# Optimization experiments

Measured on AMD Instinct MI355X. Metric: run time of the kernel, lower is better.

## Reference

```python
import jax, jax.numpy as jnp
import numpy as np

B = 16384      # batch
IN = 512       # input width
G, F, O = 64, 24, 16      # hidden: groups, fan_in, group_out (width = G*O = 1024)
GO_G, GO_F, GO_O = 4, 48, 16  # output layer: 4 groups x 16 = 64 outputs


def setup_inputs() -> dict:
    key = jax.random.key(0)
    ks = jax.random.split(key, 13)
    # total columns available (concat of input + all prior hidden layers)
    tot = [IN, IN + G * O, IN + 2 * G * O, IN + 3 * G * O]  # 512,1536,2560,3584
    scale = 0.1
    return {
        "x": jax.random.normal(ks[0], (B, IN), jnp.float32),
        "W1": jax.random.normal(ks[1], (G, F, O), jnp.float32) * scale,
        "b1": jnp.zeros((G, O), jnp.float32),
        "W2": jax.random.normal(ks[2], (G, F, O), jnp.float32) * scale,
        "b2": jnp.zeros((G, O), jnp.float32),
        "W3": jax.random.normal(ks[3], (G, F, O), jnp.float32) * scale,
        "b3": jnp.zeros((G, O), jnp.float32),
        "Wo": jax.random.normal(ks[4], (GO_G, GO_F, GO_O), jnp.float32) * scale,
        "bo": jnp.zeros((GO_G, GO_O), jnp.float32),
        "idx1": jax.random.randint(ks[5], (G, F), 0, tot[0], jnp.int32),
        "idx2": jax.random.randint(ks[6], (G, F), 0, tot[1], jnp.int32),
        "idx3": jax.random.randint(ks[7], (G, F), 0, tot[2], jnp.int32),
        "idxo": jax.random.randint(ks[8], (GO_G, GO_F), 0, tot[3], jnp.int32),
    }


def _group_layer(acc, idx, W, b, act):
    # acc: [B, P] concat of all prior layer outputs; idx: [G, F] column coords
    g = acc[:, idx]                               # [B, G, F] irregular gather
    h = jnp.einsum('bgf,gfo->bgo', g, W) + b      # many tiny dense sublayers
    h = act(h)
    return h.reshape(h.shape[0], -1)              # concat groups -> [B, G*O]


def reference(x, W1, b1, W2, b2, W3, b3, Wo, bo, idx1, idx2, idx3, idxo):
    acc = x
    for idx, W, b in ((idx1, W1, b1), (idx2, W2, b2), (idx3, W3, b3)):
        out = _group_layer(acc, idx, W, b, jnp.tanh)
        acc = jnp.concatenate([acc, out], axis=1)  # inputs.append(layer_out)
    # output layer uses linear out_activation
    return _group_layer(acc, idxo, Wo, bo, lambda h: h)  # [B, 64]
```

## Files before the change

### kernel.cpp

```cpp
#include <hip/hip_runtime.h>
#include <hip/hip_bf16.h>


typedef unsigned short ushort_t;
typedef unsigned int uint_t;
typedef __attribute__((ext_vector_type(8))) short short8;
typedef __attribute__((ext_vector_type(4))) float f32x4;

#define ACC_STRIDE 3588
#define ROW_BYTES (ACC_STRIDE * 2)
#define PAD_ONE 3584
#define ONE_BYTE (PAD_ONE * 2)
#define ZERO_BYTE (3586 * 2)
#define ACC_U16 (16 * ACC_STRIDE)
#define OFFS_BYTES 25600
#define LDS_BYTES (ACC_U16 * 2 + OFFS_BYTES)

#define OFF_HID_B 204800
#define OFF_HEAD_B 229376

__device__ __forceinline__ ushort_t f2bf(float f) {
    __hip_bfloat16 h = __float2bfloat16(f);
    union { __hip_bfloat16 h; ushort_t u; } v;
    v.h = h;
    return v.u;
}

__device__ __forceinline__ uint_t pack2bf(float lo, float hi) {
    return (uint_t)f2bf(lo) | ((uint_t)f2bf(hi) << 16);
}

__device__ __forceinline__ float fast_tanh(float x) {
    float e = __expf(2.0f * x);
    return fmaf(-2.0f, __builtin_amdgcn_rcpf(e + 1.0f), 1.0f);
}

__global__ __launch_bounds__(256)
void convert_weights(const float* __restrict__ W1, const float* __restrict__ b1,
                     const float* __restrict__ W2, const float* __restrict__ b2,
                     const float* __restrict__ W3, const float* __restrict__ b3,
                     const float* __restrict__ Wo, const float* __restrict__ bo,
                     const int* __restrict__ idx1, const int* __restrict__ idx2,
                     const int* __restrict__ idx3, const int* __restrict__ idxo,
                     ushort_t* __restrict__ ws)
{
    const int tid = blockIdx.x * 256 + threadIdx.x;
    const int lane = tid & 63;
    const int nn = lane & 15;
    const int quad = lane >> 4;
    if (tid < 12288) {
        const int g = (tid >> 6) & 63;
        const int l = tid >> 12;
        const float* W = (l == 0) ? W1 : (l == 1) ? W2 : W3;
        const float* bb = (l == 0) ? b1 : (l == 1) ? b2 : b3;
        const float* Wg = W + g * 384;
        ushort_t v[8];
        #pragma unroll
        for (int j = 0; j < 8; ++j) {
            const int k = quad * 8 + j;
            v[j] = (k < 24) ? f2bf(Wg[k * 16 + nn])
                 : (k == 24) ? f2bf(bb[g * 16 + nn]) : (ushort_t)0;
        }
        ushort4* dst = reinterpret_cast<ushort4*>(ws + (size_t)tid * 8);
        dst[0] = make_ushort4(v[0], v[1], v[2], v[3]);
        dst[1] = make_ushort4(v[4], v[5], v[6], v[7]);
    } else if (tid < 12800) {
        const int h = tid - 12288;
        const int gs = h >> 6;
        const int go = gs >> 1;
        const int step = gs & 1;
        const float* Wg = Wo + go * 768;
        ushort_t v[8];
        #pragma unroll
        for (int j = 0; j < 8; ++j) {
            const int k = step * 32 + quad * 8 + j;
            v[j] = (k < 48) ? f2bf(Wg[k * 16 + nn])
                 : (k == 48) ? f2bf(bo[go * 16 + nn]) : (ushort_t)0;
        }
        ushort4* dst = reinterpret_cast<ushort4*>(ws + (size_t)tid * 8);
        dst[0] = make_ushort4(v[0], v[1], v[2], v[3]);
        dst[1] = make_ushort4(v[4], v[5], v[6], v[7]);
    } else if (tid < 18944) {
        const int e = tid - 12800;
        const int l = e >> 11;
        const int rem = e & 2047;
        const int g = rem >> 5;
        const int k = rem & 31;
        const int* idx = (l == 0) ? idx1 : (l == 1) ? idx2 : idx3;
        const int v = (k < 24) ? idx[g * 24 + k] * 2
                    : (k == 24) ? ONE_BYTE : ZERO_BYTE;
        reinterpret_cast<int*>((char*)ws + OFF_HID_B)[e] = v;
    } else if (tid < 19200) {
        const int e = tid - 18944;
        const int go = e >> 6;
        const int k = e & 63;
        const int v = (k < 48) ? idxo[go * 48 + k] * 2
                    : (k == 48) ? ONE_BYTE : ZERO_BYTE;
        reinterpret_cast<int*>((char*)ws + OFF_HEAD_B)[e] = v;
    }
}

#define NTILES 4

__global__ __launch_bounds__(1024)
void demodel_mfma(const float* __restrict__ x,
                  const ushort_t* __restrict__ ws,
                  float* __restrict__ out)
{
    extern __shared__ __align__(16) ushort_t smem[];
    const int t = threadIdx.x;
    const int lane = t & 63;
    const int wv = t >> 6;
    const int nn = lane & 15;
    const int quad = lane >> 4;

    {
        const uint4* src = reinterpret_cast<const uint4*>((const char*)ws + OFF_HID_B);
        uint4* dst = reinterpret_cast<uint4*>(smem + ACC_U16);
        for (int i = t; i < OFFS_BYTES / 16; i += 1024)
            dst[i] = src[i];
    }
    if (t < 16) {
        uint2* p = reinterpret_cast<uint2*>((char*)smem + t * ROW_BYTES + ONE_BYTE);
        *p = make_uint2(0x00003f80u, 0u);
    }

    const int* offs = reinterpret_cast<const int*>(smem + ACC_U16);
    const char* accb = (const char*)smem + nn * ROW_BYTES;
    char* accw = (char*)smem;

    const int pr = (t - 512) >> 5;
    const int pc = (t & 31) << 4;
    uint_t px[8];

    if (wv >= 8) {
        const float4* src = reinterpret_cast<const float4*>(
            x + ((size_t)blockIdx.x * 16 + pr) * 512 + pc);
        float4 a0 = src[0], a1 = src[1], a2 = src[2], a3 = src[3];
        px[0] = pack2bf(a0.x, a0.y); px[1] = pack2bf(a0.z, a0.w);
        px[2] = pack2bf(a1.x, a1.y); px[3] = pack2bf(a1.z, a1.w);
        px[4] = pack2bf(a2.x, a2.y); px[5] = pack2bf(a2.z, a2.w);
        px[6] = pack2bf(a3.x, a3.y); px[7] = pack2bf(a3.z, a3.w);
    }

    #pragma unroll 1
    for (int it = 0; it < NTILES; ++it) {
        const int row0 = (it * 256 + blockIdx.x) * 16;

        __syncthreads();
        if (wv >= 8) {
            uint2* d = reinterpret_cast<uint2*>(accw + pr * ROW_BYTES + pc * 2);
            d[0] = make_uint2(px[0], px[1]);
            d[1] = make_uint2(px[2], px[3]);
            d[2] = make_uint2(px[4], px[5]);
            d[3] = make_uint2(px[6], px[7]);
        }
        __syncthreads();

        #pragma unroll 1
        for (int l = 0; l < 3; ++l) {
            const int out_base = 512 + l * 1024;
            const int g0 = wv << 2;

            int4 o0[4], o1[4];
            short8 bfr[4];
            #pragma unroll
            for (int gi = 0; gi < 4; ++gi) {
                const int* op = offs + l * 2048 + (g0 + gi) * 32 + quad * 8;
                o0[gi] = *reinterpret_cast<const int4*>(op);
                o1[gi] = *reinterpret_cast<const int4*>(op + 4);
                bfr[gi] = *reinterpret_cast<const short8*>(
                    ws + (((size_t)l * 64 + g0 + gi) * 64 + lane) * 8);
            }

            short8 af[4];
            #pragma unroll
            for (int gi = 0; gi < 4; ++gi) {
                af[gi][0] = *(const short*)(accb + o0[gi].x);
                af[gi][1] = *(const short*)(accb + o0[gi].y);
                af[gi][2] = *(const short*)(accb + o0[gi].z);
                af[gi][3] = *(const short*)(accb + o0[gi].w);
                af[gi][4] = *(const short*)(accb + o1[gi].x);
                af[gi][5] = *(const short*)(accb + o1[gi].y);
                af[gi][6] = *(const short*)(accb + o1[gi].z);
                af[gi][7] = *(const short*)(accb + o1[gi].w);
            }

            f32x4 acc[4];
            #pragma unroll
            for (int gi = 0; gi < 4; ++gi) {
                f32x4 z = { 0.f, 0.f, 0.f, 0.f };
                acc[gi] = __builtin_amdgcn_mfma_f32_16x16x32_bf16(af[gi], bfr[gi], z, 0, 0, 0);
            }

            #pragma unroll
            for (int gi = 0; gi < 4; ++gi) {
                const int colo = out_base + (g0 + gi) * 16 + nn;
                #pragma unroll
                for (int i = 0; i < 4; ++i)
                    smem[(quad * 4 + i) * ACC_STRIDE + colo] = f2bf(fast_tanh(acc[gi][i]));
            }
            __syncthreads();
        }

        if (wv < 4) {
            const int go = wv;
            int4 o0[2], o1[2];
            short8 bfr[2];
            #pragma unroll
            for (int s = 0; s < 2; ++s) {
                const int* op = offs + 6144 + go * 64 + s * 32 + quad * 8;
                o0[s] = *reinterpret_cast<const int4*>(op);
                o1[s] = *reinterpret_cast<const int4*>(op + 4);
                bfr[s] = *reinterpret_cast<const short8*>(
                    ws + (12288 + ((size_t)go * 2 + s) * 64 + lane) * 8);
            }
            short8 af[2];
            #pragma unroll
            for (int s = 0; s < 2; ++s) {
                af[s][0] = *(const short*)(accb + o0[s].x);
                af[s][1] = *(const short*)(accb + o0[s].y);
                af[s][2] = *(const short*)(accb + o0[s].z);
                af[s][3] = *(const short*)(accb + o0[s].w);
                af[s][4] = *(const short*)(accb + o1[s].x);
                af[s][5] = *(const short*)(accb + o1[s].y);
                af[s][6] = *(const short*)(accb + o1[s].z);
                af[s][7] = *(const short*)(accb + o1[s].w);
            }
            f32x4 z = { 0.f, 0.f, 0.f, 0.f };
            f32x4 a0 = __builtin_amdgcn_mfma_f32_16x16x32_bf16(af[0], bfr[0], z, 0, 0, 0);
            f32x4 a1 = __builtin_amdgcn_mfma_f32_16x16x32_bf16(af[1], bfr[1], z, 0, 0, 0);
            #pragma unroll
            for (int i = 0; i < 4; ++i)
                out[(size_t)(row0 + quad * 4 + i) * 64 + go * 16 + nn] = a0[i] + a1[i];
        }
        if (wv >= 8 && it + 1 < NTILES) {
            const float4* src = reinterpret_cast<const float4*>(
                x + (((size_t)(it + 1) * 256 + blockIdx.x) * 16 + pr) * 512 + pc);
            float4 a0 = src[0], a1 = src[1], a2 = src[2], a3 = src[3];
            px[0] = pack2bf(a0.x, a0.y); px[1] = pack2bf(a0.z, a0.w);
            px[2] = pack2bf(a1.x, a1.y); px[3] = pack2bf(a1.z, a1.w);
            px[4] = pack2bf(a2.x, a2.y); px[5] = pack2bf(a2.z, a2.w);
            px[6] = pack2bf(a3.x, a3.y); px[7] = pack2bf(a3.z, a3.w);
        }
    }
}

extern "C" void kernel_launch(void* const* d_in, const int* in_sizes, int n_in,
                              void* d_out, int out_size, void* d_ws, size_t ws_size,
                              hipStream_t stream) {
    const float* x  = (const float*)d_in[0];
    const float* W1 = (const float*)d_in[1];
    const float* b1 = (const float*)d_in[2];
    const float* W2 = (const float*)d_in[3];
    const float* b2 = (const float*)d_in[4];
    const float* W3 = (const float*)d_in[5];
    const float* b3 = (const float*)d_in[6];
    const float* Wo = (const float*)d_in[7];
    const float* bo = (const float*)d_in[8];
    const int* idx1 = (const int*)d_in[9];
    const int* idx2 = (const int*)d_in[10];
    const int* idx3 = (const int*)d_in[11];
    const int* idxo = (const int*)d_in[12];
    float* out = (float*)d_out;

    (void)hipFuncSetAttribute((const void*)demodel_mfma,
                              hipFuncAttributeMaxDynamicSharedMemorySize,
                              LDS_BYTES);

    convert_weights<<<75, 256, 0, stream>>>(W1, b1, W2, b2, W3, b3, Wo, bo,
                                            idx1, idx2, idx3, idxo,
                                            (ushort_t*)d_ws);

    demodel_mfma<<<256, 1024, LDS_BYTES, stream>>>(
        x, (const ushort_t*)d_ws, out);
}
```

Before: 123.2 us.

## Swap MFMA operands for vectorized stores and read gather offsets from global

The MFMA A/B operands are swapped, so the accumulator comes out transposed. Each lane then holds four consecutive output columns of one row and can write them as a packed 8-byte LDS store and a float4 global store, instead of four scalar stores. The per-block copy of the gather offset table into LDS is also removed; offsets are now read directly from global memory through the cache. This saves LDS space and the startup copy, but the offset loads now hit L1/L2 instead of LDS.

```diff
diff --git a/kernel.cpp b/kernel.cpp
--- a/kernel.cpp
+++ b/kernel.cpp
@@ -13,8 +13,7 @@
 #define ONE_BYTE (PAD_ONE * 2)
 #define ZERO_BYTE (3586 * 2)
 #define ACC_U16 (16 * ACC_STRIDE)
-#define OFFS_BYTES 25600
-#define LDS_BYTES (ACC_U16 * 2 + OFFS_BYTES)
+#define LDS_BYTES (ACC_U16 * 2)
 
 #define OFF_HID_B 204800
 #define OFF_HEAD_B 229376
@@ -114,18 +113,13 @@
     const int nn = lane & 15;
     const int quad = lane >> 4;
 
-    {
-        const uint4* src = reinterpret_cast<const uint4*>((const char*)ws + OFF_HID_B);
-        uint4* dst = reinterpret_cast<uint4*>(smem + ACC_U16);
-        for (int i = t; i < OFFS_BYTES / 16; i += 1024)
-            dst[i] = src[i];
-    }
+    const int* offs = reinterpret_cast<const int*>((const char*)ws + OFF_HID_B);
+
     if (t < 16) {
         uint2* p = reinterpret_cast<uint2*>((char*)smem + t * ROW_BYTES + ONE_BYTE);
         *p = make_uint2(0x00003f80u, 0u);
     }
 
-    const int* offs = reinterpret_cast<const int*>(smem + ACC_U16);
     const char* accb = (const char*)smem + nn * ROW_BYTES;
     char* accw = (char*)smem;
 
@@ -190,15 +184,16 @@
             #pragma unroll
             for (int gi = 0; gi < 4; ++gi) {
                 f32x4 z = { 0.f, 0.f, 0.f, 0.f };
-                acc[gi] = __builtin_amdgcn_mfma_f32_16x16x32_bf16(af[gi], bfr[gi], z, 0, 0, 0);
-            }
-
-            #pragma unroll
-            for (int gi = 0; gi < 4; ++gi) {
-                const int colo = out_base + (g0 + gi) * 16 + nn;
-                #pragma unroll
-                for (int i = 0; i < 4; ++i)
-                    smem[(quad * 4 + i) * ACC_STRIDE + colo] = f2bf(fast_tanh(acc[gi][i]));
+                acc[gi] = __builtin_amdgcn_mfma_f32_16x16x32_bf16(bfr[gi], af[gi], z, 0, 0, 0);
+            }
+
+            #pragma unroll
+            for (int gi = 0; gi < 4; ++gi) {
+                const int colo = out_base + (g0 + gi) * 16 + quad * 4;
+                uint2 w = make_uint2(
+                    pack2bf(fast_tanh(acc[gi][0]), fast_tanh(acc[gi][1])),
+                    pack2bf(fast_tanh(acc[gi][2]), fast_tanh(acc[gi][3])));
+                *reinterpret_cast<uint2*>(accw + nn * ROW_BYTES + colo * 2) = w;
             }
             __syncthreads();
         }
@@ -228,11 +223,15 @@
                 af[s][7] = *(const short*)(accb + o1[s].w);
             }
             f32x4 z = { 0.f, 0.f, 0.f, 0.f };
-            f32x4 a0 = __builtin_amdgcn_mfma_f32_16x16x32_bf16(af[0], bfr[0], z, 0, 0, 0);
-            f32x4 a1 = __builtin_amdgcn_mfma_f32_16x16x32_bf16(af[1], bfr[1], z, 0, 0, 0);
-            #pragma unroll
-            for (int i = 0; i < 4; ++i)
-                out[(size_t)(row0 + quad * 4 + i) * 64 + go * 16 + nn] = a0[i] + a1[i];
+            f32x4 a0 = __builtin_amdgcn_mfma_f32_16x16x32_bf16(bfr[0], af[0], z, 0, 0, 0);
+            f32x4 a1 = __builtin_amdgcn_mfma_f32_16x16x32_bf16(bfr[1], af[1], z, 0, 0, 0);
+            float4 o;
+            o.x = a0[0] + a1[0];
+            o.y = a0[1] + a1[1];
+            o.z = a0[2] + a1[2];
+            o.w = a0[3] + a1[3];
+            *reinterpret_cast<float4*>(
+                out + (size_t)(row0 + nn) * 64 + go * 16 + quad * 4) = o;
         }
         if (wv >= 8 && it + 1 < NTILES) {
             const float4* src = reinterpret_cast<const float4*>(
```

Result: slower. 128.2 us (+4.0%).
